# Performance work log

Measured on AMD Instinct MI355X. Metric: run time of the kernel, lower is better.

Reference implementation:

```python
import jax, jax.numpy as jnp
import numpy as np

N = 1_000_000
C = 32
GRID_SIZE = (16, 16, 16, 16, 16)

# Only 4 corners are combined in the original module: dims 0 and 1 vary
# between floor/ceil, dims 2-4 always use floor.
CORNER_OFFSETS = np.array([
    [0, 0, 0, 0, 0],
    [1, 0, 0, 0, 0],
    [0, 1, 0, 0, 0],
    [1, 1, 0, 0, 0],
], dtype=np.int32)  # (4, 5)


def setup_inputs() -> dict:
    key = jax.random.key(0)
    k1, k2 = jax.random.split(key)
    ray = jax.random.uniform(k1, (N, 5), dtype=jnp.float32)
    grid = jax.random.normal(k2, (1, C) + GRID_SIZE, dtype=jnp.float32)
    ray_min = jnp.zeros((5,), dtype=jnp.float32)
    ray_max = jnp.ones((5,), dtype=jnp.float32)
    return {"ray": ray, "grid": grid, "ray_min": ray_min, "ray_max": ray_max}


def reference(ray, grid, ray_min, ray_max):
    dims = np.array(grid.shape[2:], dtype=np.int64)       # (D0..D4)
    C_ = grid.shape[1]
    P = int(np.prod(dims))
    strides = np.array([np.prod(dims[i + 1:]) for i in range(5)], dtype=np.int32)  # (5,)

    # Normalize ray -> fractional grid coordinates, shape (N, 5)
    ind = (ray - ray_min) / (ray_max - ray_min) * (dims.astype(np.float32) - 1.0)
    bottom = jnp.floor(ind).astype(jnp.int32)              # (N, 5)
    w = ind - bottom.astype(ind.dtype)                     # (N, 5) interp weights

    offs = jnp.asarray(CORNER_OFFSETS)                     # (4, 5)
    corner = bottom[None, :, :] + offs[:, None, :]         # (4, N, 5)

    dims_j = jnp.asarray(dims.astype(np.int32))
    valid = jnp.all((corner >= 0) & (corner < dims_j), axis=-1)          # (4, N)
    lin = jnp.sum(corner * jnp.asarray(strides), axis=-1)                # (4, N)
    lin = jnp.clip(lin, 0, P - 1)

    # Per-corner multilinear weights: pick w where offset==1 else (1-w), product over 5 dims
    wsel = jnp.where(offs[:, None, :] == 1, w[None, :, :], 1.0 - w[None, :, :])  # (4, N, 5)
    comb_w = jnp.prod(wsel, axis=-1) * valid.astype(ind.dtype)                   # (4, N)

    grid_flat = grid.reshape(C_, P)                        # (C, P)
    vals = grid_flat[:, lin]                               # (C, 4, N) gather
    out = jnp.einsum('cfn,fn->nc', vals, comb_w)           # (N, C)
    return out
```

## Files before the change

kernel.cpp:

```cpp
#include <hip/hip_runtime.h>
#include <hip/hip_fp16.h>

#define PCELLS (16*16*16*16*16)
#define CCH 32
#define TILE_P 128

typedef float f32x4 __attribute__((ext_vector_type(4)));

__device__ __forceinline__ float swz_xor4(float x) {
    return __int_as_float(__builtin_amdgcn_ds_swizzle(__float_as_int(x), 0x101F));
}

__device__ __forceinline__ void ray_base2(
        const float* __restrict__ ray, const float* __restrict__ mn,
        const float* __restrict__ mx, int n0, int n1,
        int* l0, float* w00, float* w10, float* tau0,
        int* l1, float* w01, float* w11, float* tau1) {
    float wa[5], wb[5]; int ba[5], bb[5];
#pragma unroll
    for (int d = 0; d < 5; ++d) {
        float m   = mn[d];
        float inv = __builtin_amdgcn_rcpf(mx[d] - m) * 15.0f;
        float i0  = (ray[(size_t)n0 * 5 + d] - m) * inv;
        float i1  = (ray[(size_t)n1 * 5 + d] - m) * inv;
        float f0 = floorf(i0), f1 = floorf(i1);
        ba[d] = (int)f0;  wa[d] = i0 - f0;
        bb[d] = (int)f1;  wb[d] = i1 - f1;
    }
    *tau0 = (1.f - wa[2]) * (1.f - wa[3]) * (1.f - wa[4]);
    *tau1 = (1.f - wb[2]) * (1.f - wb[3]) * (1.f - wb[4]);
    int ra = ba[2] * 256 + ba[3] * 16 + ba[4];
    int rb = bb[2] * 256 + bb[3] * 16 + bb[4];
    int la = ra * 256 + ba[0] * 16 + ba[1];
    int lb = rb * 256 + bb[0] * 16 + bb[1];
    *l0 = min(max(la, 0), PCELLS - 18);
    *l1 = min(max(lb, 0), PCELLS - 18);
    *w00 = wa[0]; *w10 = wa[1];
    *w01 = wb[0]; *w11 = wb[1];
}

__global__ __launch_bounds__(256) void transpose_kernel(
        const float* __restrict__ g, __half* __restrict__ gt) {
    __shared__ float tile[CCH][TILE_P + 4];
    const int p0  = blockIdx.x * TILE_P;
    const int d01 = blockIdx.x >> 5;
    const int rb  = (blockIdx.x & 31) * TILE_P;
    const int t   = threadIdx.x;

#pragma unroll
    for (int i = 0; i < 4; ++i) {
        int idx = t + i * 256;
        int c   = idx >> 5;
        int q   = idx & 31;
        const f32x4 v = __builtin_nontemporal_load(
            (const f32x4*)(g + (size_t)c * PCELLS + p0 + 4 * q));
        *(f32x4*)&tile[c][4 * q] = v;
    }
    __syncthreads();

#pragma unroll
    for (int i = 0; i < 2; ++i) {
        int idx = t + i * 256;
        int p   = idx >> 2;
        int k   = idx & 3;
        __half2 h[4];
#pragma unroll
        for (int j = 0; j < 4; ++j)
            h[j] = __floats2half2_rn(tile[8 * k + 2 * j][p],
                                     tile[8 * k + 2 * j + 1][p]);
        size_t cell = (size_t)(rb + p) * 256 + d01;
        *(f32x4*)(gt + cell * CCH + 8 * k) = *(f32x4*)h;
    }
}

__global__ __launch_bounds__(256) void fused_gather(
        const float* __restrict__ ray, const __half* __restrict__ gt,
        const float* __restrict__ mn, const float* __restrict__ mx,
        float* __restrict__ out, int N) {
    int tid  = blockIdx.x * blockDim.x + threadIdx.x;
    int lane = tid & 63;
    int wv   = tid >> 6;
    int gi   = lane >> 3;
    int j    = lane & 7;
    int n0   = wv * 16 + gi;
    if (n0 >= N) return;
    int  n1   = n0 + 8;
    bool has1 = n1 < N;
    int  n1c  = has1 ? n1 : n0;

    int l0, l1; float w00, w10, ta, w01, w11, tb;
    ray_base2(ray, mn, mx, n0, n1c, &l0, &w00, &w10, &ta, &l1, &w01, &w11, &tb);

    const char* gb = (const char*)gt;
    const size_t off = (size_t)16 * j;
    f32x4 vA0 = *(const f32x4*)(gb + (size_t)l0 * 64 + off);
    f32x4 vB0 = *(const f32x4*)(gb + (size_t)(l0 + 16) * 64 + off);
    f32x4 vA1 = *(const f32x4*)(gb + (size_t)l1 * 64 + off);
    f32x4 vB1 = *(const f32x4*)(gb + (size_t)(l1 + 16) * 64 + off);

    const int h = j >> 2;
    float f10 = h ? w10 : 1.f - w10;
    float cA0 = (1.f - w00) * ta * f10;
    float cB0 = w00 * ta * f10;
    float f11 = h ? w11 : 1.f - w11;
    float cA1 = (1.f - w01) * tb * f11;
    float cB1 = w01 * tb * f11;

    float acc0[8], acc1[8];
    const __half2* hA0 = (const __half2*)&vA0;
    const __half2* hB0 = (const __half2*)&vB0;
    const __half2* hA1 = (const __half2*)&vA1;
    const __half2* hB1 = (const __half2*)&vB1;
#pragma unroll
    for (int k = 0; k < 4; ++k) {
        float2 a0 = __half22float2(hA0[k]);
        float2 b0 = __half22float2(hB0[k]);
        acc0[2 * k]     = cA0 * a0.x + cB0 * b0.x;
        acc0[2 * k + 1] = cA0 * a0.y + cB0 * b0.y;
        float2 a1 = __half22float2(hA1[k]);
        float2 b1 = __half22float2(hB1[k]);
        acc1[2 * k]     = cA1 * a1.x + cB1 * b1.x;
        acc1[2 * k + 1] = cA1 * a1.y + cB1 * b1.y;
    }
#pragma unroll
    for (int k = 0; k < 8; ++k) {
        acc0[k] += swz_xor4(acc0[k]);
        acc1[k] += swz_xor4(acc1[k]);
    }

    const int qo = j & 3;
    f32x4 lo0 = *(f32x4*)&acc0[0], hi0 = *(f32x4*)&acc0[4];
    f32x4 st0 = h ? hi0 : lo0;
    __builtin_nontemporal_store(
        st0, (f32x4*)(out + (size_t)n0 * CCH + 8 * qo + 4 * h));
    if (has1) {
        f32x4 lo1 = *(f32x4*)&acc1[0], hi1 = *(f32x4*)&acc1[4];
        f32x4 st1 = h ? hi1 : lo1;
        __builtin_nontemporal_store(
            st1, (f32x4*)(out + (size_t)n1 * CCH + 8 * qo + 4 * h));
    }
}

__device__ __forceinline__ void ray_corners_orig(
        const float* __restrict__ ray, const float* __restrict__ mn,
        const float* __restrict__ mx, int n, int* lin, float* wt) {
    float w[5]; int b[5];
#pragma unroll
    for (int d = 0; d < 5; ++d) {
        float m   = mn[d];
        float inv = __builtin_amdgcn_rcpf(mx[d] - m) * 15.0f;
        float i0  = (ray[(size_t)n * 5 + d] - m) * inv;
        float f0  = floorf(i0);
        b[d] = (int)f0;  w[d] = i0 - f0;
    }
    float tau = (1.f - w[2]) * (1.f - w[3]) * (1.f - w[4]);
    int rest  = b[2] * 256 + b[3] * 16 + b[4];
    wt[0] = (1.f - w[0]) * (1.f - w[1]) * tau;
    wt[1] = w[0] * (1.f - w[1]) * tau;
    wt[2] = (1.f - w[0]) * w[1] * tau;
    wt[3] = w[0] * w[1] * tau;
    int l00 = b[0] * 65536 + b[1] * 4096 + rest;
    int lv[4] = { l00, l00 + 65536, l00 + 4096, l00 + 65536 + 4096 };
#pragma unroll
    for (int f = 0; f < 4; ++f)
        lin[f] = min(max(lv[f], 0), PCELLS - 1);
}

__global__ __launch_bounds__(256) void direct_kernel(
        const float* __restrict__ ray, const float* __restrict__ g,
        const float* __restrict__ mn, const float* __restrict__ mx,
        float* __restrict__ out, int N) {
    int tid = blockIdx.x * blockDim.x + threadIdx.x;
    int n = tid >> 5;
    int c = tid & 31;
    if (n >= N) return;
    int lin[4]; float wt[4];
    ray_corners_orig(ray, mn, mx, n, lin, wt);
    const float* gc = g + (size_t)c * PCELLS;
    float acc = wt[0] * gc[lin[0]] + wt[1] * gc[lin[1]] +
                wt[2] * gc[lin[2]] + wt[3] * gc[lin[3]];
    out[(size_t)n * CCH + c] = acc;
}

extern "C" void kernel_launch(void* const* d_in, const int* in_sizes, int n_in,
                              void* d_out, int out_size, void* d_ws, size_t ws_size,
                              hipStream_t stream) {
    const float* ray  = (const float*)d_in[0];
    const float* grid = (const float*)d_in[1];
    const float* mn   = (const float*)d_in[2];
    const float* mx   = (const float*)d_in[3];
    float* out = (float*)d_out;
    const int N = in_sizes[0] / 5;

    const size_t gt_bytes = (size_t)PCELLS * CCH * sizeof(__half);

    if (ws_size >= gt_bytes) {
        __half* gt = (__half*)d_ws;
        transpose_kernel<<<PCELLS / TILE_P, 256, 0, stream>>>(grid, gt);

        long long waves   = ((long long)N + 15) / 16;
        long long threads = waves * 64;
        fused_gather<<<(int)((threads + 255) / 256), 256, 0, stream>>>(
            ray, gt, mn, mx, out, N);
    } else {
        long long total = (long long)N * CCH;
        direct_kernel<<<(int)((total + 255) / 256), 256, 0, stream>>>(
            ray, grid, mn, mx, out, N);
    }
}
```

Baseline: 297.5 us.

## Process four rays per lane group and share ray coordinates via bpermute

```diff
diff --git a/kernel.cpp b/kernel.cpp
--- a/kernel.cpp
+++ b/kernel.cpp
@@ -9,34 +9,6 @@
 
 __device__ __forceinline__ float swz_xor4(float x) {
     return __int_as_float(__builtin_amdgcn_ds_swizzle(__float_as_int(x), 0x101F));
-}
-
-__device__ __forceinline__ void ray_base2(
-        const float* __restrict__ ray, const float* __restrict__ mn,
-        const float* __restrict__ mx, int n0, int n1,
-        int* l0, float* w00, float* w10, float* tau0,
-        int* l1, float* w01, float* w11, float* tau1) {
-    float wa[5], wb[5]; int ba[5], bb[5];
-#pragma unroll
-    for (int d = 0; d < 5; ++d) {
-        float m   = mn[d];
-        float inv = __builtin_amdgcn_rcpf(mx[d] - m) * 15.0f;
-        float i0  = (ray[(size_t)n0 * 5 + d] - m) * inv;
-        float i1  = (ray[(size_t)n1 * 5 + d] - m) * inv;
-        float f0 = floorf(i0), f1 = floorf(i1);
-        ba[d] = (int)f0;  wa[d] = i0 - f0;
-        bb[d] = (int)f1;  wb[d] = i1 - f1;
-    }
-    *tau0 = (1.f - wa[2]) * (1.f - wa[3]) * (1.f - wa[4]);
-    *tau1 = (1.f - wb[2]) * (1.f - wb[3]) * (1.f - wb[4]);
-    int ra = ba[2] * 256 + ba[3] * 16 + ba[4];
-    int rb = bb[2] * 256 + bb[3] * 16 + bb[4];
-    int la = ra * 256 + ba[0] * 16 + ba[1];
-    int lb = rb * 256 + bb[0] * 16 + bb[1];
-    *l0 = min(max(la, 0), PCELLS - 18);
-    *l1 = min(max(lb, 0), PCELLS - 18);
-    *w00 = wa[0]; *w10 = wa[1];
-    *w01 = wb[0]; *w11 = wb[1];
 }
 
 __global__ __launch_bounds__(256) void transpose_kernel(
@@ -69,7 +41,8 @@
             h[j] = __floats2half2_rn(tile[8 * k + 2 * j][p],
                                      tile[8 * k + 2 * j + 1][p]);
         size_t cell = (size_t)(rb + p) * 256 + d01;
-        *(f32x4*)(gt + cell * CCH + 8 * k) = *(f32x4*)h;
+        __builtin_nontemporal_store(*(f32x4*)h,
+                                    (f32x4*)(gt + cell * CCH + 8 * k));
     }
 }
 
@@ -82,62 +55,84 @@
     int wv   = tid >> 6;
     int gi   = lane >> 3;
     int j    = lane & 7;
-    int n0   = wv * 16 + gi;
-    if (n0 >= N) return;
-    int  n1   = n0 + 8;
-    bool has1 = n1 < N;
-    int  n1c  = has1 ? n1 : n0;
-
-    int l0, l1; float w00, w10, ta, w01, w11, tb;
-    ray_base2(ray, mn, mx, n0, n1c, &l0, &w00, &w10, &ta, &l1, &w01, &w11, &tb);
+    long long base = (long long)wv * 32;
+    if (base >= N) return;
+
+    const int jd = j < 5 ? j : 4;
+    float m_d   = mn[jd];
+    float inv_d = __builtin_amdgcn_rcpf(mx[jd] - m_d) * 15.0f;
+
+    int n[4]; bool has[4];
+#pragma unroll
+    for (int r = 0; r < 4; ++r) {
+        int nr = (int)base + r * 8 + gi;
+        has[r] = nr < N;
+        n[r]   = has[r] ? nr : (N - 1);
+    }
+
+    float x[4][5];
+#pragma unroll
+    for (int r = 0; r < 4; ++r) {
+        float rv = ray[(size_t)n[r] * 5 + jd];
+        int xi = __float_as_int((rv - m_d) * inv_d);
+#pragma unroll
+        for (int d = 0; d < 5; ++d)
+            x[r][d] = __int_as_float(
+                __builtin_amdgcn_ds_bpermute(4 * (gi * 8 + d), xi));
+    }
+
+    const int h = j >> 2;
+    int   l[4];
+    float cA[4], cB[4];
+#pragma unroll
+    for (int r = 0; r < 4; ++r) {
+        float w[5]; int b[5];
+#pragma unroll
+        for (int d = 0; d < 5; ++d) {
+            float f = floorf(x[r][d]);
+            b[d] = (int)f;
+            w[d] = x[r][d] - f;
+        }
+        float tau = (1.f - w[2]) * (1.f - w[3]) * (1.f - w[4]);
+        int lr = (b[2] * 256 + b[3] * 16 + b[4]) * 256 + b[0] * 16 + b[1];
+        l[r] = min(max(lr, 0), PCELLS - 18);
+        float f1 = h ? w[1] : 1.f - w[1];
+        cA[r] = (1.f - w[0]) * tau * f1;
+        cB[r] = w[0] * tau * f1;
+    }
 
     const char* gb = (const char*)gt;
     const size_t off = (size_t)16 * j;
-    f32x4 vA0 = *(const f32x4*)(gb + (size_t)l0 * 64 + off);
-    f32x4 vB0 = *(const f32x4*)(gb + (size_t)(l0 + 16) * 64 + off);
-    f32x4 vA1 = *(const f32x4*)(gb + (size_t)l1 * 64 + off);
-    f32x4 vB1 = *(const f32x4*)(gb + (size_t)(l1 + 16) * 64 + off);
-
-    const int h = j >> 2;
-    float f10 = h ? w10 : 1.f - w10;
-    float cA0 = (1.f - w00) * ta * f10;
-    float cB0 = w00 * ta * f10;
-    float f11 = h ? w11 : 1.f - w11;
-    float cA1 = (1.f - w01) * tb * f11;
-    float cB1 = w01 * tb * f11;
-
-    float acc0[8], acc1[8];
-    const __half2* hA0 = (const __half2*)&vA0;
-    const __half2* hB0 = (const __half2*)&vB0;
-    const __half2* hA1 = (const __half2*)&vA1;
-    const __half2* hB1 = (const __half2*)&vB1;
-#pragma unroll
-    for (int k = 0; k < 4; ++k) {
-        float2 a0 = __half22float2(hA0[k]);
-        float2 b0 = __half22float2(hB0[k]);
-        acc0[2 * k]     = cA0 * a0.x + cB0 * b0.x;
-        acc0[2 * k + 1] = cA0 * a0.y + cB0 * b0.y;
-        float2 a1 = __half22float2(hA1[k]);
-        float2 b1 = __half22float2(hB1[k]);
-        acc1[2 * k]     = cA1 * a1.x + cB1 * b1.x;
-        acc1[2 * k + 1] = cA1 * a1.y + cB1 * b1.y;
-    }
-#pragma unroll
-    for (int k = 0; k < 8; ++k) {
-        acc0[k] += swz_xor4(acc0[k]);
-        acc1[k] += swz_xor4(acc1[k]);
+    f32x4 vA[4], vB[4];
+#pragma unroll
+    for (int r = 0; r < 4; ++r) {
+        vA[r] = *(const f32x4*)(gb + (size_t)l[r] * 64 + off);
+        vB[r] = *(const f32x4*)(gb + (size_t)(l[r] + 16) * 64 + off);
     }
 
     const int qo = j & 3;
-    f32x4 lo0 = *(f32x4*)&acc0[0], hi0 = *(f32x4*)&acc0[4];
-    f32x4 st0 = h ? hi0 : lo0;
-    __builtin_nontemporal_store(
-        st0, (f32x4*)(out + (size_t)n0 * CCH + 8 * qo + 4 * h));
-    if (has1) {
-        f32x4 lo1 = *(f32x4*)&acc1[0], hi1 = *(f32x4*)&acc1[4];
-        f32x4 st1 = h ? hi1 : lo1;
-        __builtin_nontemporal_store(
-            st1, (f32x4*)(out + (size_t)n1 * CCH + 8 * qo + 4 * h));
+#pragma unroll
+    for (int r = 0; r < 4; ++r) {
+        float acc[8];
+        const __half2* hA = (const __half2*)&vA[r];
+        const __half2* hB = (const __half2*)&vB[r];
+#pragma unroll
+        for (int k = 0; k < 4; ++k) {
+            float2 a = __half22float2(hA[k]);
+            float2 bvl = __half22float2(hB[k]);
+            acc[2 * k]     = cA[r] * a.x + cB[r] * bvl.x;
+            acc[2 * k + 1] = cA[r] * a.y + cB[r] * bvl.y;
+        }
+#pragma unroll
+        for (int k = 0; k < 8; ++k)
+            acc[k] += swz_xor4(acc[k]);
+
+        if (has[r]) {
+            f32x4 lo = *(f32x4*)&acc[0], hi = *(f32x4*)&acc[4];
+            f32x4 st = h ? hi : lo;
+            __builtin_nontemporal_store(
+                st, (f32x4*)(out + (size_t)n[r] * CCH + 8 * qo + 4 * h));
+        }
     }
 }
 
@@ -198,7 +193,7 @@
         __half* gt = (__half*)d_ws;
         transpose_kernel<<<PCELLS / TILE_P, 256, 0, stream>>>(grid, gt);
 
-        long long waves   = ((long long)N + 15) / 16;
+        long long waves   = ((long long)N + 31) / 32;
         long long threads = waves * 64;
         fused_gather<<<(int)((threads + 255) / 256), 256, 0, stream>>>(
             ray, gt, mn, mx, out, N);
```

Measured after the change: 303.8 us. +2.1%, slower.
